# Kernel optimization log

Hardware: AMD Instinct MI355X
Metric: run time of the kernel (lower is better)

The kernel has to match this reference:

```python
import jax, jax.numpy as jnp
from jax import lax
import numpy as np

V, D_MODEL, N_LAYER, D_STATE, D_CONV, EXPAND = 32000, 1024, 2, 16, 4, 2
D_INNER = EXPAND * D_MODEL          # 2048
DT_RANK = D_MODEL // 16             # 64 (ceil(d_model/16) in mamba_ssm)
B, L = 2, 2048


def setup_inputs() -> dict:
    key = jax.random.key(0)
    ks = jax.random.split(key, 10)
    f = lambda k, shape, s=0.02: (jax.random.normal(k, shape) * s).astype(jnp.float32)
    return {
        "tokens": jax.random.randint(ks[0], (B, L), 0, V),
        "embedding": f(ks[1], (V, D_MODEL)),
        "in_proj_w": f(ks[2], (N_LAYER, 2 * D_INNER, D_MODEL)),
        "conv_w": f(ks[3], (N_LAYER, D_INNER, D_CONV), 0.2),
        "conv_b": jnp.zeros((N_LAYER, D_INNER), jnp.float32),
        "x_proj_w": f(ks[4], (N_LAYER, DT_RANK + 2 * D_STATE, D_INNER)),
        "dt_proj_w": f(ks[5], (N_LAYER, D_INNER, DT_RANK), 0.1),
        "dt_proj_b": f(ks[6], (N_LAYER, D_INNER), 0.5),
        # S4D-real init: A_log = log(1..d_state), A = -exp(A_log)
        "A_log": jnp.tile(jnp.log(jnp.arange(1, D_STATE + 1, dtype=jnp.float32))[None, None, :], (N_LAYER, D_INNER, 1)),
        "D_skip": jnp.ones((N_LAYER, D_INNER), jnp.float32),
        "out_proj_w": f(ks[7], (N_LAYER, D_MODEL, D_INNER)),
        "norm_gamma": jnp.ones((D_MODEL,), jnp.float32),
        "norm_beta": jnp.zeros((D_MODEL,), jnp.float32),
        "lm_head_w": f(ks[8], (V, D_MODEL)),
    }


def _causal_dw_conv(x, w, b):
    # x: [B,L,C], w: [C,K] depthwise causal conv (kernel K=4)
    K = w.shape[1]
    xp = jnp.pad(x, ((0, 0), (K - 1, 0), (0, 0)))
    y = sum(xp[:, k:k + x.shape[1], :] * w[:, k] for k in range(K))
    return y + b


def _mamba_block(x, in_w, cw, cb, xp_w, dt_w, dt_b, A_log, D_skip, out_w):
    # in_proj -> split into u (ssm branch) and z (gate)
    xz = jnp.einsum('bld,ed->ble', x, in_w)          # [B,L,2*d_inner]
    u, z = jnp.split(xz, 2, axis=-1)
    u = jax.nn.silu(_causal_dw_conv(u, cw, cb))      # [B,L,d_inner]
    x_dbl = jnp.einsum('ble,re->blr', u, xp_w)       # [B,L,dt_rank+2*d_state]
    dt, B_ssm, C_ssm = jnp.split(x_dbl, [DT_RANK, DT_RANK + D_STATE], axis=-1)
    delta = jax.nn.softplus(jnp.einsum('blr,er->ble', dt, dt_w) + dt_b)  # [B,L,d_inner]
    A = -jnp.exp(A_log)                              # [d_inner,d_state]

    def step(h, inp):
        u_t, d_t, b_t, c_t = inp                     # [B,e],[B,e],[B,s],[B,s]
        h = h * jnp.exp(d_t[:, :, None] * A) + (d_t * u_t)[:, :, None] * b_t[:, None, :]
        y = jnp.einsum('bes,bs->be', h, c_t)
        return h, y

    h0 = jnp.zeros((u.shape[0], D_INNER, D_STATE), u.dtype)
    _, ys = lax.scan(step, h0, (u.swapaxes(0, 1), delta.swapaxes(0, 1),
                                B_ssm.swapaxes(0, 1), C_ssm.swapaxes(0, 1)))
    y = ys.swapaxes(0, 1) + u * D_skip               # D skip connection
    y = y * jax.nn.silu(z)                           # gating
    return jnp.einsum('ble,de->bld', y, out_w)


def reference(tokens, embedding, in_proj_w, conv_w, conv_b, x_proj_w, dt_proj_w,
              dt_proj_b, A_log, D_skip, out_proj_w, norm_gamma, norm_beta, lm_head_w):
    x = embedding[tokens]                            # [B,L,d_model]
    for i in range(N_LAYER):
        x = _mamba_block(x, in_proj_w[i], conv_w[i], conv_b[i], x_proj_w[i],
                         dt_proj_w[i], dt_proj_b[i], A_log[i], D_skip[i], out_proj_w[i])
    mu = jnp.mean(x, axis=-1, keepdims=True)
    var = jnp.mean(jnp.square(x - mu), axis=-1, keepdims=True)
    xn = (x - mu) * lax.rsqrt(var + 1e-5) * norm_gamma + norm_beta
    return jnp.einsum('bld,vd->blv', xn, lm_head_w)  # logits [B,L,V]
```

## Files before the change

kernel.cpp:

```cpp
#include <hip/hip_runtime.h>
#include <hip/hip_bf16.h>

#define L_SEQ 2048
#define BATCH 2
#define DM    1024
#define DI    2048
#define DS    16
#define DTR   64
#define DBLC  96
#define VOCAB 32000
#define BL    (BATCH * L_SEQ)
#define NCH   32
#define CHL   (L_SEQ / NCH)
#define EL    8

typedef unsigned short u16;
typedef short s8v  __attribute__((ext_vector_type(8)));
typedef float f32x4 __attribute__((ext_vector_type(4)));

typedef __attribute__((address_space(1))) const void* as1cv;
typedef __attribute__((address_space(3))) void*       as3v;

static __device__ __forceinline__ u16 f2bf(float f) {
    unsigned u = __builtin_bit_cast(unsigned, f);
    u += 0x7fffu + ((u >> 16) & 1u);
    return (u16)(u >> 16);
}

__global__ __launch_bounds__(256) void cvt_bf16_kernel(
    const float* __restrict__ in, u16* __restrict__ out, int n8)
{
    int i = blockIdx.x * 256 + threadIdx.x;
    if (i >= n8) return;
    const float4* p = (const float4*)in + 2 * (size_t)i;
    float4 a = p[0], b = p[1];
    s8v o;
    o[0] = (short)f2bf(a.x); o[1] = (short)f2bf(a.y);
    o[2] = (short)f2bf(a.z); o[3] = (short)f2bf(a.w);
    o[4] = (short)f2bf(b.x); o[5] = (short)f2bf(b.y);
    o[6] = (short)f2bf(b.z); o[7] = (short)f2bf(b.w);
    ((s8v*)out)[i] = o;
}

__global__ __launch_bounds__(256) void cvt2_bf16_kernel(
    const float* __restrict__ inA, u16* __restrict__ outA, int n8A,
    const float* __restrict__ inB, u16* __restrict__ outB, int n8B)
{
    int i = blockIdx.x * 256 + threadIdx.x;
    const float* src; u16* dst; int idx;
    if (i < n8A) { src = inA; dst = outA; idx = i; }
    else if (i < n8A + n8B) { src = inB; dst = outB; idx = i - n8A; }
    else return;
    const float4* p = (const float4*)src + 2 * (size_t)idx;
    float4 a = p[0], b = p[1];
    s8v o;
    o[0] = (short)f2bf(a.x); o[1] = (short)f2bf(a.y);
    o[2] = (short)f2bf(a.z); o[3] = (short)f2bf(a.w);
    o[4] = (short)f2bf(b.x); o[5] = (short)f2bf(b.y);
    o[6] = (short)f2bf(b.z); o[7] = (short)f2bf(b.w);
    ((s8v*)dst)[idx] = o;
}

__global__ __launch_bounds__(256) void embed_kernel(
    const int* __restrict__ tok, const float* __restrict__ emb,
    u16* __restrict__ Xb)
{
    int row = blockIdx.x;
    int t = tok[row];
    float4 v = ((const float4*)(emb + (size_t)t * DM))[threadIdx.x];
    ushort4 o;
    o.x = f2bf(v.x); o.y = f2bf(v.y); o.z = f2bf(v.z); o.w = f2bf(v.w);
    ((ushort4*)(Xb + (size_t)row * DM))[threadIdx.x] = o;
}

template<int MODE>
__global__ __launch_bounds__(256) void gemm_bb(
    const u16* __restrict__ A, int lda,
    const u16* __restrict__ Bt, int ldb,
    float* __restrict__ C0, float* __restrict__ C1,
    u16* __restrict__ Cb, int ldc0, int K)
{
    __shared__ __align__(16) u16 As[2][128 * 32];
    __shared__ __align__(16) u16 Bs[2][128 * 32];

    const int tid  = threadIdx.x;
    const int lane = tid & 63;
    const int wv   = tid >> 6;
    const int bm = blockIdx.x * 128;
    const int bn = blockIdx.y * 128;

    const int ks = (lane & 3) ^ ((lane >> 3) & 3);
    const int sr = wv * 32 + (lane >> 2);
    const u16* ag0 = A  + (size_t)(bm + sr) * lda + ks * 8;
    const u16* ag1 = ag0 + 16 * (size_t)lda;
    const u16* bg0 = Bt + (size_t)(bn + sr) * ldb + ks * 8;
    const u16* bg1 = bg0 + 16 * (size_t)ldb;
    const int lo0 = wv * 1024;
    const int lo1 = wv * 1024 + 512;

    const int li = lane & 15;
    const int kc = lane >> 4;
    const int wr = (wv >> 1) * 64;
    const int wc = (wv & 1) * 64;
    const int fo = (kc ^ ((li >> 1) & 3)) * 8;

    f32x4 acc[4][4];
#pragma unroll
    for (int m = 0; m < 4; ++m)
#pragma unroll
        for (int n = 0; n < 4; ++n) acc[m][n] = (f32x4)0.f;

#define STAGE(buf, kk)                                                         \
    do {                                                                       \
        __builtin_amdgcn_global_load_lds((as1cv)(ag0 + (kk)),                  \
            (as3v)&As[buf][lo0], 16, 0, 0);                                    \
        __builtin_amdgcn_global_load_lds((as1cv)(ag1 + (kk)),                  \
            (as3v)&As[buf][lo1], 16, 0, 0);                                    \
        __builtin_amdgcn_global_load_lds((as1cv)(bg0 + (kk)),                  \
            (as3v)&Bs[buf][lo0], 16, 0, 0);                                    \
        __builtin_amdgcn_global_load_lds((as1cv)(bg1 + (kk)),                  \
            (as3v)&Bs[buf][lo1], 16, 0, 0);                                    \
    } while (0)

    const int nt = K >> 5;
    STAGE(0, 0);
    asm volatile("s_waitcnt vmcnt(0)" ::: "memory");
    __builtin_amdgcn_s_barrier();
    __builtin_amdgcn_sched_barrier(0);

    int cur = 0;
    for (int t = 0; t < nt; ++t) {
        if (t + 1 < nt) STAGE(cur ^ 1, (t + 1) << 5);

        const u16* Ab = &As[cur][0];
        const u16* Bb = &Bs[cur][0];
        s8v af[4], bf[4];
#pragma unroll
        for (int m = 0; m < 4; ++m)
            af[m] = *(const s8v*)&Ab[(wr + m * 16 + li) * 32 + fo];
#pragma unroll
        for (int n = 0; n < 4; ++n)
            bf[n] = *(const s8v*)&Bb[(wc + n * 16 + li) * 32 + fo];
#pragma unroll
        for (int m = 0; m < 4; ++m)
#pragma unroll
            for (int n = 0; n < 4; ++n)
                acc[m][n] = __builtin_amdgcn_mfma_f32_16x16x32_bf16(
                    af[m], bf[n], acc[m][n], 0, 0, 0);

        if (t + 1 < nt) {
            asm volatile("s_waitcnt vmcnt(0)" ::: "memory");
            __builtin_amdgcn_s_barrier();
            __builtin_amdgcn_sched_barrier(0);
            cur ^= 1;
        }
    }
#undef STAGE

#pragma unroll
    for (int m = 0; m < 4; ++m) {
#pragma unroll
        for (int j = 0; j < 4; ++j) {
            int row = bm + wr + m * 16 + kc * 4 + j;
#pragma unroll
            for (int n = 0; n < 4; ++n) {
                int col = bn + wc + n * 16 + li;
                float v = acc[m][n][j];
                if (MODE == 0) {
                    C0[(size_t)row * ldc0 + col] = v;
                } else if (MODE == 1) {
                    if (bn < DI) C0[(size_t)row * DI + col] = v;
                    else         C1[(size_t)row * DI + col - DI] = v;
                } else {
                    C0[(size_t)row * ldc0 + col] = v;
                    Cb[(size_t)row * ldc0 + col] = f2bf(v);
                }
            }
        }
    }
}

template<int EPI, bool NGUARD, bool SPLITK>
__global__ __launch_bounds__(256) void sgemm_bt(
    const float* __restrict__ A, int lda,
    const float* __restrict__ Bt, int ldb,
    float* __restrict__ C, int ldc,
    const float* __restrict__ bias,
    int M, int N, int K, int kchunk)
{
    __shared__ float As[16][132];
    __shared__ float Bs[16][132];

    const int tid = threadIdx.x;
    const int bm = blockIdx.y * 128;
    const int bn = blockIdx.x * 128;

    int k0 = 0, kend = K;
    if (SPLITK) {
        k0 = blockIdx.z * kchunk;
        kend = k0 + kchunk; if (kend > K) kend = K;
        C += (size_t)blockIdx.z * (size_t)M * (size_t)ldc;
    }

    const int tx = tid & 15;
    const int ty = tid >> 4;
    const int lr = tid >> 2;
    const int lc = (tid & 3) << 2;

    float acc[8][8];
#pragma unroll
    for (int i = 0; i < 8; ++i)
#pragma unroll
        for (int j = 0; j < 8; ++j) acc[i][j] = 0.f;

    for (int kk = k0; kk < kend; kk += 16) {
#pragma unroll
        for (int p = 0; p < 2; ++p) {
            int r = lr + p * 64;
            float4 v = *(const float4*)(A + (size_t)(bm + r) * lda + kk + lc);
            As[lc + 0][r] = v.x; As[lc + 1][r] = v.y;
            As[lc + 2][r] = v.z; As[lc + 3][r] = v.w;
        }
#pragma unroll
        for (int p = 0; p < 2; ++p) {
            int r = lr + p * 64;
            float4 v = make_float4(0.f, 0.f, 0.f, 0.f);
            if (!NGUARD || (bn + r) < N)
                v = *(const float4*)(Bt + (size_t)(bn + r) * ldb + kk + lc);
            Bs[lc + 0][r] = v.x; Bs[lc + 1][r] = v.y;
            Bs[lc + 2][r] = v.z; Bs[lc + 3][r] = v.w;
        }
        __syncthreads();
#pragma unroll
        for (int k = 0; k < 16; ++k) {
            float4 a0 = *(const float4*)&As[k][ty * 4];
            float4 a1 = *(const float4*)&As[k][64 + ty * 4];
            float4 b0 = *(const float4*)&Bs[k][tx * 4];
            float4 b1 = *(const float4*)&Bs[k][64 + tx * 4];
            float av[8] = {a0.x, a0.y, a0.z, a0.w, a1.x, a1.y, a1.z, a1.w};
            float bv[8] = {b0.x, b0.y, b0.z, b0.w, b1.x, b1.y, b1.z, b1.w};
#pragma unroll
            for (int i = 0; i < 8; ++i)
#pragma unroll
                for (int j = 0; j < 8; ++j)
                    acc[i][j] += av[i] * bv[j];
        }
        __syncthreads();
    }

#pragma unroll
    for (int p = 0; p < 2; ++p) {
#pragma unroll
        for (int ii = 0; ii < 4; ++ii) {
            int row = bm + p * 64 + ty * 4 + ii;
#pragma unroll
            for (int q = 0; q < 2; ++q) {
                int col = bn + q * 64 + tx * 4;
                if (NGUARD && col >= N) continue;
                float4 v;
                float* vp = &v.x;
#pragma unroll
                for (int jj = 0; jj < 4; ++jj) {
                    float x = acc[p * 4 + ii][q * 4 + jj];
                    if (EPI == 1) {
                        x += bias[col + jj];
                        x = (x > 20.f) ? x : log1pf(__expf(x));
                    }
                    vp[jj] = x;
                }
                *(float4*)(C + (size_t)row * ldc + col) = v;
            }
        }
    }
}

__global__ __launch_bounds__(256) void reduce8_kernel(
    const float* __restrict__ part, float* __restrict__ out, int n)
{
    int i = blockIdx.x * 256 + threadIdx.x;
    if (i < n) {
        float s = 0.f;
#pragma unroll
        for (int j = 0; j < 8; ++j) s += part[(size_t)j * n + i];
        out[i] = s;
    }
}

__global__ __launch_bounds__(256) void conv_silu_kernel(
    const float* __restrict__ XZu, const float* __restrict__ cw,
    const float* __restrict__ cb, float* __restrict__ U)
{
    int idx = blockIdx.x * 256 + threadIdx.x;
    int c4 = idx & 511;
    int row = idx >> 9;
    int t = row & (L_SEQ - 1);
    int c = c4 << 2;

    float4 acc;
    acc.x = cb[c]; acc.y = cb[c + 1]; acc.z = cb[c + 2]; acc.w = cb[c + 3];
    float4 w0 = *(const float4*)(cw + (size_t)(c + 0) * 4);
    float4 w1 = *(const float4*)(cw + (size_t)(c + 1) * 4);
    float4 w2 = *(const float4*)(cw + (size_t)(c + 2) * 4);
    float4 w3 = *(const float4*)(cw + (size_t)(c + 3) * 4);
#pragma unroll
    for (int k = 0; k < 4; ++k) {
        int tt = t - 3 + k;
        if (tt >= 0) {
            float4 xv = *(const float4*)(XZu + (size_t)(row - 3 + k) * DI + c);
            acc.x += xv.x * ((&w0.x)[k]);
            acc.y += xv.y * ((&w1.x)[k]);
            acc.z += xv.z * ((&w2.x)[k]);
            acc.w += xv.w * ((&w3.x)[k]);
        }
    }
    acc.x = acc.x / (1.f + __expf(-acc.x));
    acc.y = acc.y / (1.f + __expf(-acc.y));
    acc.z = acc.z / (1.f + __expf(-acc.z));
    acc.w = acc.w / (1.f + __expf(-acc.w));
    *(float4*)(U + (size_t)row * DI + c) = acc;
}

__global__ __launch_bounds__(256) void scan_fused(
    const float* __restrict__ U, const float* __restrict__ DELTA,
    const float* __restrict__ DBL, const float* __restrict__ ZF,
    const float* __restrict__ A_log, const float* __restrict__ Dskip,
    u16* __restrict__ Yb)
{
    __shared__ float ps[EL][NCH][DS][2];
    __shared__ float hs[EL][NCH][DS];

    const int tid   = threadIdx.x;
    const int el    = tid & (EL - 1);
    const int chunk = tid >> 3;
    const int bid   = blockIdx.x;
    const int b     = bid >> 8;
    const int e     = (bid & 255) * EL + el;
    const int t0    = chunk * CHL;

    float Ae[DS];
#pragma unroll
    for (int s = 0; s < DS; ++s)
        Ae[s] = -__expf(A_log[(size_t)e * DS + s]);

    const float* up = U     + (size_t)b * L_SEQ * DI + e;
    const float* dp = DELTA + (size_t)b * L_SEQ * DI + e;
    const float* zp = ZF    + (size_t)b * L_SEQ * DI + e;
    const float* bp = DBL   + ((size_t)b * L_SEQ + t0) * DBLC + DTR;
    const float* cp = bp + DS;
    u16* yp = Yb + (size_t)b * L_SEQ * DI + e;

    float P[DS], S[DS];
#pragma unroll
    for (int s = 0; s < DS; ++s) { P[s] = 1.f; S[s] = 0.f; }

    {
        float u0 = up[(size_t)t0 * DI];
        float d0 = dp[(size_t)t0 * DI];
        float4 B0[4];
#pragma unroll
        for (int q = 0; q < 4; ++q) B0[q] = *(const float4*)(bp + q * 4);

        for (int i = 0; i < CHL; ++i) {
            float u1 = 0.f, d1 = 0.f;
            float4 B1[4] = {};
            if (i + 1 < CHL) {
                u1 = up[(size_t)(t0 + i + 1) * DI];
                d1 = dp[(size_t)(t0 + i + 1) * DI];
#pragma unroll
                for (int q = 0; q < 4; ++q)
                    B1[q] = *(const float4*)(bp + (i + 1) * DBLC + q * 4);
            }
            float du = d0 * u0;
            const float* Bf = (const float*)&B0[0];
#pragma unroll
            for (int s = 0; s < DS; ++s) {
                float a = __expf(d0 * Ae[s]);
                P[s] *= a;
                S[s] = S[s] * a + du * Bf[s];
            }
            u0 = u1; d0 = d1;
#pragma unroll
            for (int q = 0; q < 4; ++q) B0[q] = B1[q];
        }
    }
#pragma unroll
    for (int s = 0; s < DS; ++s) {
        ps[el][chunk][s][0] = P[s];
        ps[el][chunk][s][1] = S[s];
    }
    __syncthreads();

    if (tid < EL * DS) {
        int pel = tid >> 4;
        int s   = tid & 15;
        float h = 0.f;
#pragma unroll
        for (int c = 0; c < NCH; ++c) {
            hs[pel][c][s] = h;
            h = ps[pel][c][s][0] * h + ps[pel][c][s][1];
        }
    }
    __syncthreads();

    float Dk = Dskip[e];
    float h[DS];
#pragma unroll
    for (int s = 0; s < DS; ++s) h[s] = hs[el][chunk][s];

    {
        float u0 = up[(size_t)t0 * DI];
        float d0 = dp[(size_t)t0 * DI];
        float z0 = zp[(size_t)t0 * DI];
        float4 B0[4], C0[4];
#pragma unroll
        for (int q = 0; q < 4; ++q) {
            B0[q] = *(const float4*)(bp + q * 4);
            C0[q] = *(const float4*)(cp + q * 4);
        }

        for (int i = 0; i < CHL; ++i) {
            float u1 = 0.f, d1 = 0.f, z1 = 0.f;
            float4 B1[4] = {}, C1[4] = {};
            if (i + 1 < CHL) {
                u1 = up[(size_t)(t0 + i + 1) * DI];
                d1 = dp[(size_t)(t0 + i + 1) * DI];
                z1 = zp[(size_t)(t0 + i + 1) * DI];
#pragma unroll
                for (int q = 0; q < 4; ++q) {
                    B1[q] = *(const float4*)(bp + (i + 1) * DBLC + q * 4);
                    C1[q] = *(const float4*)(cp + (i + 1) * DBLC + q * 4);
                }
            }
            float du = d0 * u0;
            const float* Bf = (const float*)&B0[0];
            const float* Cf = (const float*)&C0[0];
            float y0 = 0.f, y1 = 0.f, y2 = 0.f, y3 = 0.f;
#pragma unroll
            for (int s = 0; s < DS; ++s) {
                float a = __expf(d0 * Ae[s]);
                h[s] = h[s] * a + du * Bf[s];
                float hc = h[s] * Cf[s];
                if ((s & 3) == 0) y0 += hc;
                else if ((s & 3) == 1) y1 += hc;
                else if ((s & 3) == 2) y2 += hc;
                else y3 += hc;
            }
            float p = (y0 + y1) + (y2 + y3);
            float g = z0 / (1.f + __expf(-z0));
            yp[(size_t)(t0 + i) * DI] = f2bf((p + u0 * Dk) * g);
            u0 = u1; d0 = d1; z0 = z1;
#pragma unroll
            for (int q = 0; q < 4; ++q) { B0[q] = B1[q]; C0[q] = C1[q]; }
        }
    }
}

__global__ __launch_bounds__(256) void layernorm_kernel(
    const float* __restrict__ X, const float* __restrict__ g,
    const float* __restrict__ be, u16* __restrict__ XNb)
{
    __shared__ float red[4];
    int row = blockIdx.x;
    int tid = threadIdx.x;
    float4 v = ((const float4*)(X + (size_t)row * DM))[tid];

    float ssum = v.x + v.y + v.z + v.w;
#pragma unroll
    for (int o = 32; o >= 1; o >>= 1) ssum += __shfl_xor(ssum, o);
    if ((tid & 63) == 0) red[tid >> 6] = ssum;
    __syncthreads();
    float mean = (red[0] + red[1] + red[2] + red[3]) * (1.f / DM);
    __syncthreads();

    float dx = v.x - mean, dy = v.y - mean, dz = v.z - mean, dw = v.w - mean;
    float sq = dx * dx + dy * dy + dz * dz + dw * dw;
#pragma unroll
    for (int o = 32; o >= 1; o >>= 1) sq += __shfl_xor(sq, o);
    if ((tid & 63) == 0) red[tid >> 6] = sq;
    __syncthreads();
    float var = (red[0] + red[1] + red[2] + red[3]) * (1.f / DM);
    float rs = rsqrtf(var + 1e-5f);

    float4 gv = ((const float4*)g)[tid];
    float4 bv = ((const float4*)be)[tid];
    ushort4 o;
    o.x = f2bf(dx * rs * gv.x + bv.x);
    o.y = f2bf(dy * rs * gv.y + bv.y);
    o.z = f2bf(dz * rs * gv.z + bv.z);
    o.w = f2bf(dw * rs * gv.w + bv.w);
    ((ushort4*)(XNb + (size_t)row * DM))[tid] = o;
}

extern "C" void kernel_launch(void* const* d_in, const int* in_sizes, int n_in,
                              void* d_out, int out_size, void* d_ws, size_t ws_size,
                              hipStream_t stream)
{
    const int*   tokens = (const int*)d_in[0];
    const float* emb    = (const float*)d_in[1];
    const float* in_w   = (const float*)d_in[2];
    const float* conv_w = (const float*)d_in[3];
    const float* conv_b = (const float*)d_in[4];
    const float* xp_w   = (const float*)d_in[5];
    const float* dt_w   = (const float*)d_in[6];
    const float* dt_b   = (const float*)d_in[7];
    const float* A_log  = (const float*)d_in[8];
    const float* Dskip  = (const float*)d_in[9];
    const float* out_w  = (const float*)d_in[10];
    const float* gamma  = (const float*)d_in[11];
    const float* beta   = (const float*)d_in[12];
    const float* lm_w   = (const float*)d_in[13];
    float* out = (float*)d_out;

    float* ws = (float*)d_ws;
    size_t off = 0;
    float* X     = ws + off; off += (size_t)BL * DM;
    float* XZu   = ws + off; off += (size_t)BL * DI;
    float* U     = ws + off; off += (size_t)BL * DI;
    float* ZF    = ws + off; off += (size_t)BL * DI;
    float* DELTA = ws + off; off += (size_t)BL * DI;
    float* DBL   = ws + off; off += (size_t)BL * DBLC;
    u16* Xb     = (u16*)(ws + off); off += (size_t)BL * DM / 2;
    u16* wb_in  = (u16*)(ws + off); off += (size_t)2 * DI * DM / 2;
    u16* wb_out = (u16*)(ws + off); off += (size_t)DM * DI / 2;
    u16* Yb    = (u16*)XZu;
    u16* wb_lm = (u16*)XZu;
    float* PART = DELTA;
    u16* XNb   = Xb;

    embed_kernel<<<BL, 256, 0, stream>>>(tokens, emb, Xb);

    const int SCAN_GRID = BATCH * (DI / EL);

    for (int l = 0; l < 2; ++l) {
        const float* cwp = conv_w + (size_t)l * DI * 4;
        const float* cbp = conv_b + (size_t)l * DI;
        const float* xw  = xp_w   + (size_t)l * DBLC * DI;
        const float* dw  = dt_w   + (size_t)l * DI * DTR;
        const float* dbp = dt_b   + (size_t)l * DI;
        const float* alp = A_log  + (size_t)l * DI * DS;
        const float* dkp = Dskip  + (size_t)l * DI;

        const int n8i = 2 * DI * DM / 8, n8o = DM * DI / 8;
        cvt2_bf16_kernel<<<(n8i + n8o + 255) / 256, 256, 0, stream>>>(
            in_w + (size_t)l * 2 * DI * DM, wb_in, n8i,
            out_w + (size_t)l * DM * DI, wb_out, n8o);

        gemm_bb<1><<<dim3(32, 32), 256, 0, stream>>>(
            Xb, DM, wb_in, DM, XZu, ZF, nullptr, 0, DM);
        conv_silu_kernel<<<(BL * DI / 4) / 256, 256, 0, stream>>>(XZu, cwp, cbp, U);
        sgemm_bt<0, true, true><<<dim3(1, 32, 8), 256, 0, stream>>>(
            U, DI, xw, DI, PART, DBLC, nullptr, BL, DBLC, DI, DI / 8);
        reduce8_kernel<<<(BL * DBLC + 255) / 256, 256, 0, stream>>>(
            PART, DBL, BL * DBLC);
        sgemm_bt<1, false, false><<<dim3(16, 32), 256, 0, stream>>>(
            DBL, DBLC, dw, DTR, DELTA, DI, dbp, BL, DI, DTR, 0);
        scan_fused<<<SCAN_GRID, 256, 0, stream>>>(
            U, DELTA, DBL, ZF, alp, dkp, Yb);
        gemm_bb<2><<<dim3(32, 8), 256, 0, stream>>>(
            Yb, DI, wb_out, DI, X, nullptr, Xb, DM, DI);
    }

    cvt_bf16_kernel<<<((size_t)VOCAB * DM / 8 + 255) / 256, 256, 0, stream>>>(
        lm_w, wb_lm, VOCAB * DM / 8);

    layernorm_kernel<<<BL, 256, 0, stream>>>(X, gamma, beta, XNb);

    gemm_bb<0><<<dim3(32, 250), 256, 0, stream>>>(
        XNb, DM, wb_lm, DM, out, nullptr, nullptr, VOCAB, DM);
}
```

Baseline: 1.033 ms.

## Use 256x256 tile, 512-thread GEMM with 4-stage LDS pipeline for in_proj and lm_head

Adds a gemm_deep kernel that computes 256x256 output tiles with 8 waves and a 4-buffer global_load_lds prefetch pipeline, keeping three k-slices in flight. It replaces the 128x128 double-buffered GEMM for the in_proj and lm_head multiplies, which raises operand reuse per loaded byte and hides more load latency. The out_proj GEMM moves to a separate specialised kernel. The larger tiles use 128 KB of LDS and many accumulator registers, which lowers occupancy and leaves fewer blocks for the in_proj grid.

```diff
diff --git a/kernel.cpp b/kernel.cpp
--- a/kernel.cpp
+++ b/kernel.cpp
@@ -74,11 +74,129 @@
 }
 
 template<int MODE>
-__global__ __launch_bounds__(256) void gemm_bb(
+__global__ __launch_bounds__(512) void gemm_deep(
     const u16* __restrict__ A, int lda,
     const u16* __restrict__ Bt, int ldb,
     float* __restrict__ C0, float* __restrict__ C1,
-    u16* __restrict__ Cb, int ldc0, int K)
+    int ldc0, int K)
+{
+    __shared__ __align__(16) u16 As[4][256 * 32];
+    __shared__ __align__(16) u16 Bs[4][256 * 32];
+
+    const int tid  = threadIdx.x;
+    const int lane = tid & 63;
+    const int wv   = tid >> 6;
+    const int bm = blockIdx.x * 256;
+    const int bn = blockIdx.y * 256;
+
+    const int ks = (lane & 3) ^ ((lane >> 3) & 3);
+    const int lr = lane >> 2;
+    const u16* ag0 = A  + (size_t)(bm + wv * 32 + lr) * lda + ks * 8;
+    const u16* ag1 = ag0 + 16 * (size_t)lda;
+    const u16* bg0 = Bt + (size_t)(bn + wv * 32 + lr) * ldb + ks * 8;
+    const u16* bg1 = bg0 + 16 * (size_t)ldb;
+    const int lo0 = wv * 1024;
+    const int lo1 = wv * 1024 + 512;
+
+    const int li = lane & 15;
+    const int kc = lane >> 4;
+    const int wr = (wv >> 2) * 128;
+    const int wc = (wv & 3) * 64;
+    const int fo = (kc ^ ((li >> 1) & 3)) * 8;
+
+    f32x4 acc[8][4];
+#pragma unroll
+    for (int m = 0; m < 8; ++m)
+#pragma unroll
+        for (int n = 0; n < 4; ++n) acc[m][n] = (f32x4)0.f;
+
+#define STG(buf, kk)                                                           \
+    do {                                                                       \
+        __builtin_amdgcn_global_load_lds((as1cv)(ag0 + (kk)),                  \
+            (as3v)&As[buf][lo0], 16, 0, 0);                                    \
+        __builtin_amdgcn_global_load_lds((as1cv)(ag1 + (kk)),                  \
+            (as3v)&As[buf][lo1], 16, 0, 0);                                    \
+        __builtin_amdgcn_global_load_lds((as1cv)(bg0 + (kk)),                  \
+            (as3v)&Bs[buf][lo0], 16, 0, 0);                                    \
+        __builtin_amdgcn_global_load_lds((as1cv)(bg1 + (kk)),                  \
+            (as3v)&Bs[buf][lo1], 16, 0, 0);                                    \
+    } while (0)
+
+    const int nt = K >> 5;
+    STG(0, 0);
+    STG(1, 32);
+    STG(2, 64);
+    asm volatile("s_waitcnt vmcnt(8)" ::: "memory");
+    __builtin_amdgcn_s_barrier();
+    __builtin_amdgcn_sched_barrier(0);
+
+    for (int t = 0; t < nt; ++t) {
+        if (t + 3 < nt) STG((t + 3) & 3, (t + 3) << 5);
+
+        const u16* Ab = &As[t & 3][0];
+        const u16* Bb = &Bs[t & 3][0];
+        s8v af[8], bf[4];
+#pragma unroll
+        for (int m = 0; m < 8; ++m)
+            af[m] = *(const s8v*)&Ab[(wr + m * 16 + li) * 32 + fo];
+#pragma unroll
+        for (int n = 0; n < 4; ++n)
+            bf[n] = *(const s8v*)&Bb[(wc + n * 16 + li) * 32 + fo];
+
+        __builtin_amdgcn_s_setprio(1);
+#pragma unroll
+        for (int m = 0; m < 4; ++m)
+#pragma unroll
+            for (int n = 0; n < 4; ++n)
+                acc[m][n] = __builtin_amdgcn_mfma_f32_16x16x32_bf16(
+                    af[m], bf[n], acc[m][n], 0, 0, 0);
+        __builtin_amdgcn_s_setprio(0);
+        __builtin_amdgcn_s_setprio(1);
+#pragma unroll
+        for (int m = 4; m < 8; ++m)
+#pragma unroll
+            for (int n = 0; n < 4; ++n)
+                acc[m][n] = __builtin_amdgcn_mfma_f32_16x16x32_bf16(
+                    af[m], bf[n], acc[m][n], 0, 0, 0);
+        __builtin_amdgcn_s_setprio(0);
+
+        if (t + 1 < nt) {
+            if (t + 3 < nt)
+                asm volatile("s_waitcnt vmcnt(8)" ::: "memory");
+            else if (t + 2 < nt)
+                asm volatile("s_waitcnt vmcnt(4)" ::: "memory");
+            else
+                asm volatile("s_waitcnt vmcnt(0)" ::: "memory");
+            __builtin_amdgcn_s_barrier();
+            __builtin_amdgcn_sched_barrier(0);
+        }
+    }
+#undef STG
+
+#pragma unroll
+    for (int m = 0; m < 8; ++m) {
+#pragma unroll
+        for (int j = 0; j < 4; ++j) {
+            int row = bm + wr + m * 16 + kc * 4 + j;
+#pragma unroll
+            for (int n = 0; n < 4; ++n) {
+                int col = bn + wc + n * 16 + li;
+                float v = acc[m][n][j];
+                if (MODE == 0) {
+                    C0[(size_t)row * ldc0 + col] = v;
+                } else {
+                    if (bn < DI) C0[(size_t)row * DI + col] = v;
+                    else         C1[(size_t)row * DI + col - DI] = v;
+                }
+            }
+        }
+    }
+}
+
+__global__ __launch_bounds__(256) void gemm_bb2(
+    const u16* __restrict__ A, int lda,
+    const u16* __restrict__ Bt, int ldb,
+    float* __restrict__ C0, u16* __restrict__ Cb, int ldc0, int K)
 {
     __shared__ __align__(16) u16 As[2][128 * 32];
     __shared__ __align__(16) u16 Bs[2][128 * 32];
@@ -166,15 +284,8 @@
             for (int n = 0; n < 4; ++n) {
                 int col = bn + wc + n * 16 + li;
                 float v = acc[m][n][j];
-                if (MODE == 0) {
-                    C0[(size_t)row * ldc0 + col] = v;
-                } else if (MODE == 1) {
-                    if (bn < DI) C0[(size_t)row * DI + col] = v;
-                    else         C1[(size_t)row * DI + col - DI] = v;
-                } else {
-                    C0[(size_t)row * ldc0 + col] = v;
-                    Cb[(size_t)row * ldc0 + col] = f2bf(v);
-                }
+                C0[(size_t)row * ldc0 + col] = v;
+                Cb[(size_t)row * ldc0 + col] = f2bf(v);
             }
         }
     }
@@ -545,8 +656,8 @@
             in_w + (size_t)l * 2 * DI * DM, wb_in, n8i,
             out_w + (size_t)l * DM * DI, wb_out, n8o);
 
-        gemm_bb<1><<<dim3(32, 32), 256, 0, stream>>>(
-            Xb, DM, wb_in, DM, XZu, ZF, nullptr, 0, DM);
+        gemm_deep<1><<<dim3(16, 16), 512, 0, stream>>>(
+            Xb, DM, wb_in, DM, XZu, ZF, 0, DM);
         conv_silu_kernel<<<(BL * DI / 4) / 256, 256, 0, stream>>>(XZu, cwp, cbp, U);
         sgemm_bt<0, true, true><<<dim3(1, 32, 8), 256, 0, stream>>>(
             U, DI, xw, DI, PART, DBLC, nullptr, BL, DBLC, DI, DI / 8);
@@ -556,8 +667,8 @@
             DBL, DBLC, dw, DTR, DELTA, DI, dbp, BL, DI, DTR, 0);
         scan_fused<<<SCAN_GRID, 256, 0, stream>>>(
             U, DELTA, DBL, ZF, alp, dkp, Yb);
-        gemm_bb<2><<<dim3(32, 8), 256, 0, stream>>>(
-            Yb, DI, wb_out, DI, X, nullptr, Xb, DM, DI);
+        gemm_bb2<<<dim3(32, 8), 256, 0, stream>>>(
+            Yb, DI, wb_out, DI, X, Xb, DM, DI);
     }
 
     cvt_bf16_kernel<<<((size_t)VOCAB * DM / 8 + 255) / 256, 256, 0, stream>>>(
@@ -565,6 +676,6 @@
 
     layernorm_kernel<<<BL, 256, 0, stream>>>(X, gamma, beta, XNb);
 
-    gemm_bb<0><<<dim3(32, 250), 256, 0, stream>>>(
-        XNb, DM, wb_lm, DM, out, nullptr, nullptr, VOCAB, DM);
-}
+    gemm_deep<0><<<dim3(16, 125), 512, 0, stream>>>(
+        XNb, DM, wb_lm, DM, out, nullptr, VOCAB, DM);
+}
```

Result: slower. 1.107 ms (+7.2%).
